# Kernel optimization log

Hardware: AMD Instinct MI355X
Metric: run time of the kernel (lower is better)

## Reference

```python
import jax, jax.numpy as jnp
import numpy as np


def group_norm(x, g, b, groups, eps=1e-5):
    # x: (B, C, H, W), PyTorch GroupNorm semantics
    B, C, H, W = x.shape
    xr = x.reshape(B, groups, -1)
    m = xr.mean(-1, keepdims=True)
    v = xr.var(-1, keepdims=True)
    xn = ((xr - m) * jax.lax.rsqrt(v + eps)).reshape(B, C, H, W)
    return xn * g[:, None, None] + b[:, None, None]


def mamba(xs, in_w, conv_w, conv_b, xproj_w, dt_w, dt_b, A_log, D, out_w):
    # Standard Mamba block: in_proj -> causal depthwise conv -> SiLU ->
    # x_proj -> softplus(dt_proj) -> selective scan -> gate -> out_proj.
    Bsz, L, d = xs.shape
    di = in_w.shape[0] // 2
    r = dt_w.shape[1]
    n = A_log.shape[1]
    K = conv_w.shape[1]
    xz = xs @ in_w.T                           # (B, L, 2*di)
    xpart, z = xz[..., :di], xz[..., di:]
    xp = jnp.pad(xpart, ((0, 0), (K - 1, 0), (0, 0)))  # causal pad
    xc = conv_b + sum(xp[:, k:k + L, :] * conv_w[:, k] for k in range(K))
    xc = jax.nn.silu(xc)
    proj = xc @ xproj_w.T                      # (B, L, r + 2n)
    dt = proj[..., :r]
    Bm = proj[..., r:r + n]
    Cm = proj[..., r + n:]
    delta = jax.nn.softplus(dt @ dt_w.T + dt_b)   # (B, L, di)
    A = -jnp.exp(A_log)                            # (di, n)
    dA = jnp.exp(jnp.einsum('bld,dn->bldn', delta, A))
    dBu = jnp.einsum('bld,bln,bld->bldn', delta, Bm, xc)

    def step(h, inp):
        dA_t, dBu_t, C_t = inp
        h = dA_t * h + dBu_t                  # (B, di, n)
        return h, jnp.einsum('bdn,bn->bd', h, C_t)

    h0 = jnp.zeros((Bsz, di, n), xs.dtype)
    _, ys = jax.lax.scan(step, h0, (jnp.moveaxis(dA, 1, 0), jnp.moveaxis(dBu, 1, 0), jnp.moveaxis(Cm, 1, 0)))
    y = jnp.moveaxis(ys, 0, 1) + D * xc
    y = y * jax.nn.silu(z)
    return y @ out_w.T


def setup_inputs() -> dict:
    def nrm(i, shape, s=0.05):
        return jax.random.normal(jax.random.fold_in(jax.random.key(0), i), shape, dtype=jnp.float32) * s

    f32 = jnp.float32
    C = 128
    di, r, n = 256, 8, 16          # spa mamba: d_model=128, expand=2
    di2, r2 = 64, 2                # spe mamba: d_model=32
    A1 = jnp.log(jnp.broadcast_to(jnp.arange(1, n + 1, dtype=f32), (di, n)))
    A2 = jnp.log(jnp.broadcast_to(jnp.arange(1, n + 1, dtype=f32), (di2, n)))
    return {
        'x': nrm(0, (2, C, 64, 64), 1.0),
        'pe_w': nrm(1, (C, C)), 'pe_b': jnp.zeros((C,), f32),
        'pe_gn_g': jnp.ones((C,), f32), 'pe_gn_b': jnp.zeros((C,), f32),
        'spa_in_w': nrm(2, (2 * di, C)),
        'spa_conv_w': nrm(3, (di, 4)), 'spa_conv_b': jnp.zeros((di,), f32),
        'spa_xproj_w': nrm(4, (r + 2 * n, di)),
        'spa_dt_w': nrm(5, (di, r)), 'spa_dt_b': jnp.full((di,), -2.0, f32),
        'spa_Alog': A1, 'spa_D': jnp.ones((di,), f32),
        'spa_out_w': nrm(6, (C, di)),
        'spa_gn_g': jnp.ones((C,), f32), 'spa_gn_b': jnp.zeros((C,), f32),
        'spe_in_w': nrm(7, (2 * di2, 32)),
        'spe_conv_w': nrm(8, (di2, 4)), 'spe_conv_b': jnp.zeros((di2,), f32),
        'spe_xproj_w': nrm(9, (r2 + 2 * n, di2)),
        'spe_dt_w': nrm(10, (di2, r2)), 'spe_dt_b': jnp.full((di2,), -2.0, f32),
        'spe_Alog': A2, 'spe_D': jnp.ones((di2,), f32),
        'spe_out_w': nrm(11, (32, di2)),
        'spe_gn_g': jnp.ones((C,), f32), 'spe_gn_b': jnp.zeros((C,), f32),
        'fuse_w': jnp.full((2,), 0.5, f32),
        'cls_w': nrm(12, (10, C)), 'cls_b': jnp.zeros((10,), f32),
        'ref_dw_w': nrm(13, (C, 1, 3, 3)),
        'ref_gn_g': jnp.ones((C,), f32), 'ref_gn_b': jnp.zeros((C,), f32),
        'ref_pw_w': nrm(14, (1, C)), 'ref_pw_b': jnp.zeros((1,), f32),
        'alpha': jnp.asarray(1e-4, f32),
    }


def reference(x, pe_w, pe_b, pe_gn_g, pe_gn_b, spa_in_w, spa_conv_w, spa_conv_b, spa_xproj_w, spa_dt_w, spa_dt_b, spa_Alog, spa_D, spa_out_w, spa_gn_g, spa_gn_b, spe_in_w, spe_conv_w, spe_conv_b, spe_xproj_w, spe_dt_w, spe_dt_b, spe_Alog, spe_D, spe_out_w, spe_gn_g, spe_gn_b, fuse_w, cls_w, cls_b, ref_dw_w, ref_gn_g, ref_gn_b, ref_pw_w, ref_pw_b, alpha):
    B, _, H, W = x.shape
    # patch embedding: 1x1 conv + GroupNorm + SiLU
    h1 = jnp.einsum('bchw,oc->bohw', x, pe_w) + pe_b[:, None, None]
    h1 = jax.nn.silu(group_norm(h1, pe_gn_g, pe_gn_b, 4))
    # SpaMamba: scan over flattened spatial tokens (B, H*W, C)
    seq = h1.transpose(0, 2, 3, 1).reshape(B, H * W, -1)
    y = mamba(seq, spa_in_w, spa_conv_w, spa_conv_b, spa_xproj_w, spa_dt_w, spa_dt_b, spa_Alog, spa_D, spa_out_w)
    y = y.reshape(B, H, W, -1).transpose(0, 3, 1, 2)
    spa = jax.nn.silu(group_norm(y, spa_gn_g, spa_gn_b, 4)) + h1
    # SpeMamba: token_num=4, group_channel_num=32, channel_num=128 (no pad)
    seq2 = h1.transpose(0, 2, 3, 1).reshape(B * H * W, 4, 32)
    y2 = mamba(seq2, spe_in_w, spe_conv_w, spe_conv_b, spe_xproj_w, spe_dt_w, spe_dt_b, spe_Alog, spe_D, spe_out_w)
    y2 = y2.reshape(B, H, W, -1).transpose(0, 3, 1, 2)
    spe = h1 + jax.nn.silu(group_norm(y2, spe_gn_g, spe_gn_b, 4))
    # attention-weighted fusion + residual (BothMamba, use_att=True)
    wts = jax.nn.softmax(fuse_w)
    feat = spa * wts[0] + spe * wts[1] + h1
    # classifier head (1x1 conv)
    logits = jnp.einsum('bchw,oc->bohw', feat, cls_w) + cls_b[:, None, None]
    # BoundaryAwareLogitRefiner
    edge = jax.lax.conv_general_dilated(feat, ref_dw_w, (1, 1), ((1, 1), (1, 1)), feature_group_count=feat.shape[1], dimension_numbers=('NCHW', 'OIHW', 'NCHW'))
    edge = jax.nn.silu(group_norm(edge, ref_gn_g, ref_gn_b, 4))
    edge = jax.nn.sigmoid(jnp.einsum('bchw,oc->bohw', edge, ref_pw_w) + ref_pw_b[:, None, None])
    local = jax.lax.reduce_window(logits, 0.0, jax.lax.add, (1, 1, 3, 3), (1, 1, 1, 1), ((0, 0), (0, 0), (1, 1), (1, 1))) / 9.0  # count_include_pad=True
    return logits + alpha * (1.0 - edge) * (local - logits)
```

## Files before the change

### kernel.cpp

```cpp
#include <hip/hip_runtime.h>
#include <math.h>

#define DEV __device__ __forceinline__

DEV float sigm(float x){ return 1.f/(1.f+__expf(-x)); }
DEV float siluf(float x){ return x * sigm(x); }
DEV float softplusf(float x){ return x > 20.f ? x : log1pf(__expf(x)); }

static constexpr float NG = 131072.0f;

static constexpr size_t WS_H1    = 0;
static constexpr size_t WS_H1PRE = 1048576;
static constexpr size_t WS_XC    = 2097152;
static constexpr size_t WS_ZSIL  = 4194304;
static constexpr size_t WS_XZ    = 6291456;
static constexpr size_t WS_DELTA = 6291456;
static constexpr size_t WS_BM    = 8388608;
static constexpr size_t WS_CM    = 8519680;
static constexpr size_t WS_LOG   = 8650752;
static constexpr size_t WS_Y     = 10485760;
static constexpr size_t WS_P     = 12582912;
static constexpr size_t WS_Q     = 13107200;
static constexpr size_t WS_HS    = 13631488;
static constexpr size_t WS_Y2    = 14155776;
static constexpr size_t WS_FEAT  = 15204352;
static constexpr size_t WS_STATS = 16252928;
static constexpr size_t WS_PEWT  = 16253056;
static constexpr size_t WS_INWT  = WS_PEWT  + 16384;
static constexpr size_t WS_OUTWT = WS_INWT  + 65536;
static constexpr size_t WS_XPWT  = WS_OUTWT + 32768;

__global__ void __launch_bounds__(256)
k_red(const float* __restrict__ part, float* __restrict__ outS, int half){
  __shared__ float red[4];
  int b = blockIdx.x >> 3, j = blockIdx.x & 7;
  float s = 0.f;
  for (int i = b*half + threadIdx.x; i < (b+1)*half; i += 256)
    s += part[(size_t)i*8 + j];
  s += __shfl_xor(s,1); s += __shfl_xor(s,2); s += __shfl_xor(s,4);
  s += __shfl_xor(s,8); s += __shfl_xor(s,16); s += __shfl_xor(s,32);
  if ((threadIdx.x & 63) == 0) red[threadIdx.x>>6] = s;
  __syncthreads();
  if (threadIdx.x == 0) outS[b*8+j] = red[0]+red[1]+red[2]+red[3];
}

__global__ void __launch_bounds__(256)
k_transpose(const float* __restrict__ pe_w, const float* __restrict__ in_w,
            const float* __restrict__ out_w, const float* __restrict__ xp_w,
            float* __restrict__ peT, float* __restrict__ inT,
            float* __restrict__ outT, float* __restrict__ xpT){
  int i0 = blockIdx.x*256 + threadIdx.x;
  int nt = gridDim.x*256;
  for (int k = i0; k < 128*128; k += nt){ int r = k >> 7, c = k & 127; peT[c*128 + r] = pe_w[k]; }
  for (int k = i0; k < 512*128; k += nt){ int r = k >> 7, c = k & 127; inT[c*512 + r] = in_w[k]; }
  for (int k = i0; k < 128*256; k += nt){ int r = k >> 8, c = k & 255; outT[c*128 + r] = out_w[k]; }
  for (int k = i0; k < 40*256;  k += nt){ int r = k >> 8, c = k & 255; xpT[c*40 + r] = xp_w[k]; }
}

__global__ void __launch_bounds__(256)
k_pe(const float* __restrict__ x, const float* __restrict__ peT,
     const float* __restrict__ pe_b, float* __restrict__ h1pre,
     float* __restrict__ part){
  __shared__ float As[16][36];
  __shared__ float Bs[16][64];
  __shared__ float red1[2][4], red2[2][4];
  int tid = threadIdx.x;
  int bx = blockIdx.x, by = blockIdx.y;
  int m0 = bx*32, n0 = by*64;
  int b = m0 >> 12, pl0 = m0 & 4095;
  int tx = tid & 15, ty = tid >> 4;
  float acc[2][4];
  #pragma unroll
  for (int i = 0; i < 2; i++)
    #pragma unroll
    for (int j = 0; j < 4; j++) acc[i][j] = 0.f;
  for (int k0 = 0; k0 < 128; k0 += 16){
    if (tid < 128){
      int k = tid >> 3, mm = (tid & 7)*4;
      float4 a = *(const float4*)(x + ((size_t)b*128 + k0+k)*4096 + pl0 + mm);
      *(float4*)&As[k][mm] = a;
    }
    {
      int k = tid >> 4, n = (tid & 15)*4;
      *(float4*)&Bs[k][n] = *(const float4*)(peT + (size_t)(k0+k)*128 + n0+n);
    }
    __syncthreads();
    #pragma unroll
    for (int k = 0; k < 16; k++){
      float2 av = *(const float2*)&As[k][ty*2];
      float4 bv = *(const float4*)&Bs[k][tx*4];
      acc[0][0] += av.x*bv.x; acc[0][1] += av.x*bv.y; acc[0][2] += av.x*bv.z; acc[0][3] += av.x*bv.w;
      acc[1][0] += av.y*bv.x; acc[1][1] += av.y*bv.y; acc[1][2] += av.y*bv.z; acc[1][3] += av.y*bv.w;
    }
    __syncthreads();
  }
  float4 bias = *(const float4*)(pe_b + n0 + tx*4);
  float s1 = 0.f, s2 = 0.f;
  #pragma unroll
  for (int i = 0; i < 2; i++){
    float4 st;
    st.x = acc[i][0]+bias.x; st.y = acc[i][1]+bias.y;
    st.z = acc[i][2]+bias.z; st.w = acc[i][3]+bias.w;
    s1 += st.x+st.y+st.z+st.w;
    s2 += st.x*st.x + st.y*st.y + st.z*st.z + st.w*st.w;
    *(float4*)(h1pre + (size_t)(m0 + ty*2 + i)*128 + n0 + tx*4) = st;
  }
  s1 += __shfl_xor(s1,1);  s2 += __shfl_xor(s2,1);
  s1 += __shfl_xor(s1,2);  s2 += __shfl_xor(s2,2);
  s1 += __shfl_xor(s1,4);  s2 += __shfl_xor(s2,4);
  s1 += __shfl_xor(s1,16); s2 += __shfl_xor(s2,16);
  s1 += __shfl_xor(s1,32); s2 += __shfl_xor(s2,32);
  int lane = tid & 63, w = tid >> 6;
  if ((lane & 55) == 0){
    int gl = (lane >> 3) & 1;
    red1[gl][w] = s1; red2[gl][w] = s2;
  }
  __syncthreads();
  if (tid < 8){
    int gg = tid >> 1, which = tid & 1;
    int gl = gg - by*2;
    float v = 0.f;
    if (gl == 0 || gl == 1){
      v = which ? (red2[gl][0]+red2[gl][1]+red2[gl][2]+red2[gl][3])
                : (red1[gl][0]+red1[gl][1]+red1[gl][2]+red1[gl][3]);
    }
    int pblk = b*256 + (bx & 127) + by*128;
    part[(size_t)pblk*8 + tid] = v;
  }
}

__global__ void __launch_bounds__(256)
k_gnsilu(const float* __restrict__ pre, const float* __restrict__ stats,
         const float* __restrict__ gw, const float* __restrict__ gb,
         float* __restrict__ outb){
  int idx = blockIdx.x*256 + threadIdx.x;
  int c = idx & 127; int pix = idx >> 7; int b = pix >> 12; int g = c >> 5;
  float s1 = stats[(b*4+g)*2], s2 = stats[(b*4+g)*2+1];
  float m = s1 * (1.f/NG);
  float v = s2 * (1.f/NG) - m*m;
  float xn = (pre[idx] - m) * rsqrtf(v + 1e-5f);
  float val = xn * gw[c] + gb[c];
  outb[idx] = siluf(val);
}

__global__ void __launch_bounds__(256)
k_xz(const float* __restrict__ h1, const float* __restrict__ inT,
     float* __restrict__ xz){
  __shared__ float As[16][68];
  __shared__ float Bs[16][64];
  int tid = threadIdx.x;
  int m0 = blockIdx.x*64, n0 = blockIdx.y*64;
  int tx = tid & 15, ty = tid >> 4;
  float acc[4][4];
  #pragma unroll
  for (int i = 0; i < 4; i++)
    #pragma unroll
    for (int j = 0; j < 4; j++) acc[i][j] = 0.f;
  for (int k0 = 0; k0 < 128; k0 += 16){
    {
      int m = tid >> 2, kk = (tid & 3)*4;
      float4 a = *(const float4*)(h1 + (size_t)(m0+m)*128 + k0+kk);
      As[kk+0][m] = a.x; As[kk+1][m] = a.y; As[kk+2][m] = a.z; As[kk+3][m] = a.w;
    }
    {
      int k = tid >> 4, n = (tid & 15)*4;
      *(float4*)&Bs[k][n] = *(const float4*)(inT + (size_t)(k0+k)*512 + n0+n);
    }
    __syncthreads();
    #pragma unroll
    for (int k = 0; k < 16; k++){
      float4 av = *(const float4*)&As[k][ty*4];
      float4 bv = *(const float4*)&Bs[k][tx*4];
      acc[0][0] += av.x*bv.x; acc[0][1] += av.x*bv.y; acc[0][2] += av.x*bv.z; acc[0][3] += av.x*bv.w;
      acc[1][0] += av.y*bv.x; acc[1][1] += av.y*bv.y; acc[1][2] += av.y*bv.z; acc[1][3] += av.y*bv.w;
      acc[2][0] += av.z*bv.x; acc[2][1] += av.z*bv.y; acc[2][2] += av.z*bv.z; acc[2][3] += av.z*bv.w;
      acc[3][0] += av.w*bv.x; acc[3][1] += av.w*bv.y; acc[3][2] += av.w*bv.z; acc[3][3] += av.w*bv.w;
    }
    __syncthreads();
  }
  #pragma unroll
  for (int i = 0; i < 4; i++){
    float4 st; st.x = acc[i][0]; st.y = acc[i][1]; st.z = acc[i][2]; st.w = acc[i][3];
    *(float4*)(xz + (size_t)(m0 + ty*4 + i)*512 + n0 + tx*4) = st;
  }
}

__global__ void __launch_bounds__(256)
k_conv(const float* __restrict__ xz, const float* __restrict__ cw,
       const float* __restrict__ cb, float* __restrict__ xc,
       float* __restrict__ zsil){
  int idx = blockIdx.x*256 + threadIdx.x;
  int d = idx & 255;
  int l = (idx >> 8) & 4095;
  int b = idx >> 20;
  float v = cb[d];
  #pragma unroll
  for (int k = 0; k < 4; k++){
    int ls = l - 3 + k;
    if (ls >= 0) v += xz[(size_t)(b*4096 + ls)*512 + d] * cw[d*4 + k];
  }
  xc[idx] = siluf(v);
  float z = xz[(size_t)(b*4096 + l)*512 + 256 + d];
  zsil[idx] = siluf(z);
}

__global__ void __launch_bounds__(256)
k_proj(const float* __restrict__ xc, const float* __restrict__ xpT,
       const float* __restrict__ dtw, const float* __restrict__ dtb,
       float* __restrict__ delta, float* __restrict__ Bm, float* __restrict__ Cm){
  __shared__ float xt[32][260];
  __shared__ float pr[32][40];
  int tid = threadIdx.x;
  int m0 = blockIdx.x * 32;
  for (int i = tid; i < 32*256; i += 256){
    int t = i >> 8, d = i & 255;
    xt[t][d] = xc[(size_t)(m0+t)*256 + d];
  }
  __syncthreads();
  {
    int t = tid >> 3, j0 = tid & 7;
    float a0=0.f,a1=0.f,a2=0.f,a3=0.f,a4=0.f;
    for (int d = 0; d < 256; d++){
      float xv = xt[t][d];
      const float* wp = &xpT[d*40 + j0];
      a0 += xv*wp[0]; a1 += xv*wp[8]; a2 += xv*wp[16]; a3 += xv*wp[24]; a4 += xv*wp[32];
    }
    pr[t][j0] = a0; pr[t][j0+8] = a1; pr[t][j0+16] = a2; pr[t][j0+24] = a3; pr[t][j0+32] = a4;
  }
  __syncthreads();
  {
    int d = tid;
    float w[8];
    #pragma unroll
    for (int r = 0; r < 8; r++) w[r] = dtw[d*8+r];
    float bd = dtb[d];
    for (int t = 0; t < 32; t++){
      float val = bd;
      #pragma unroll
      for (int r = 0; r < 8; r++) val += pr[t][r]*w[r];
      delta[(size_t)(m0+t)*256 + d] = softplusf(val);
    }
  }
  for (int i = tid; i < 512; i += 256){
    int t = i >> 4, n = i & 15;
    Bm[(size_t)(m0+t)*16 + n] = pr[t][8+n];
    Cm[(size_t)(m0+t)*16 + n] = pr[t][24+n];
  }
}

__global__ void __launch_bounds__(256)
k_scan1(const float* __restrict__ delta, const float* __restrict__ xc,
        const float* __restrict__ Bm, const float* __restrict__ Alog,
        float* __restrict__ P, float* __restrict__ Q){
  __shared__ float sd[64][16], sx[64][16], sb[64][16];
  int blk = blockIdx.x;
  int b = blk >> 10;
  int chunk = (blk >> 4) & 63;
  int dblk = blk & 15;
  int tid = threadIdx.x;
  size_t rowbase = (size_t)(b*4096 + chunk*64);
  for (int i = tid; i < 64*16; i += 256){
    int ii = i >> 4, dd = i & 15;
    sd[ii][dd] = delta[(rowbase + ii)*256 + dblk*16 + dd];
    sx[ii][dd] = xc  [(rowbase + ii)*256 + dblk*16 + dd];
    sb[ii][dd] = Bm  [(rowbase + ii)*16 + dd];
  }
  int dl = tid >> 4, n = tid & 15;
  int d = dblk*16 + dl;
  float An = -__expf(Alog[d*16 + n]);
  __syncthreads();
  float Pv = 1.f, Qv = 0.f;
  for (int i = 0; i < 64; i++){
    float dv = sd[i][dl];
    float a = __expf(dv * An);
    Qv = a*Qv + dv * sb[i][n] * sx[i][dl];
    Pv *= a;
  }
  size_t o = (size_t)(b*64+chunk)*4096 + dblk*256 + tid;
  P[o] = Pv; Q[o] = Qv;
}

__global__ void __launch_bounds__(256)
k_scan2(const float* __restrict__ P, const float* __restrict__ Q,
        float* __restrict__ hs){
  int gid = blockIdx.x*256 + threadIdx.x;
  int b = gid >> 12, dn = gid & 4095;
  float h = 0.f;
  for (int ch = 0; ch < 64; ch++){
    size_t idx = (size_t)(b*64 + ch)*4096 + dn;
    hs[idx] = h;
    h = P[idx]*h + Q[idx];
  }
}

__global__ void __launch_bounds__(256)
k_scan3(const float* __restrict__ delta, const float* __restrict__ xc,
        const float* __restrict__ Bm, const float* __restrict__ Cm,
        const float* __restrict__ zsil, const float* __restrict__ Alog,
        const float* __restrict__ Dv, const float* __restrict__ hs,
        float* __restrict__ y){
  __shared__ float sd[64][16], sx[64][16], sb[64][16], sc[64][16], sz[64][16], yt[64][16];
  int blk = blockIdx.x;
  int b = blk >> 10;
  int chunk = (blk >> 4) & 63;
  int dblk = blk & 15;
  int tid = threadIdx.x;
  size_t rowbase = (size_t)(b*4096 + chunk*64);
  for (int i = tid; i < 64*16; i += 256){
    int ii = i >> 4, dd = i & 15;
    sd[ii][dd] = delta[(rowbase + ii)*256 + dblk*16 + dd];
    sx[ii][dd] = xc  [(rowbase + ii)*256 + dblk*16 + dd];
    sz[ii][dd] = zsil[(rowbase + ii)*256 + dblk*16 + dd];
    sb[ii][dd] = Bm  [(rowbase + ii)*16 + dd];
    sc[ii][dd] = Cm  [(rowbase + ii)*16 + dd];
  }
  int dl = tid >> 4, n = tid & 15;
  int d = dblk*16 + dl;
  float An = -__expf(Alog[d*16 + n]);
  float h = hs[(size_t)(b*64+chunk)*4096 + dblk*256 + tid];
  float Dd = Dv[d];
  __syncthreads();
  for (int i = 0; i < 64; i++){
    float dv = sd[i][dl], xv = sx[i][dl];
    float a = __expf(dv * An);
    h = a*h + dv * sb[i][n] * xv;
    float ctr = h * sc[i][n];
    ctr += __shfl_xor(ctr, 1);
    ctr += __shfl_xor(ctr, 2);
    ctr += __shfl_xor(ctr, 4);
    ctr += __shfl_xor(ctr, 8);
    if (n == 0) yt[i][dl] = (ctr + Dd*xv) * sz[i][dl];
  }
  __syncthreads();
  for (int i = tid; i < 1024; i += 256){
    int ii = i >> 4, dd = i & 15;
    y[(rowbase + ii)*256 + dblk*16 + dd] = yt[ii][dd];
  }
}

__global__ void __launch_bounds__(256)
k_outproj(const float* __restrict__ y, const float* __restrict__ outT,
          float* __restrict__ yproj, float* __restrict__ part){
  __shared__ float As[16][36];
  __shared__ float Bs[16][64];
  __shared__ float red1[2][4], red2[2][4];
  int tid = threadIdx.x;
  int bx = blockIdx.x, by = blockIdx.y;
  int m0 = bx*32, n0 = by*64;
  int b = m0 >> 12;
  int tx = tid & 15, ty = tid >> 4;
  float acc[2][4];
  #pragma unroll
  for (int i = 0; i < 2; i++)
    #pragma unroll
    for (int j = 0; j < 4; j++) acc[i][j] = 0.f;
  for (int k0 = 0; k0 < 256; k0 += 16){
    if (tid < 128){
      int m = tid >> 2, kk = (tid & 3)*4;
      float4 a = *(const float4*)(y + (size_t)(m0+m)*256 + k0+kk);
      As[kk+0][m] = a.x; As[kk+1][m] = a.y; As[kk+2][m] = a.z; As[kk+3][m] = a.w;
    }
    {
      int k = tid >> 4, n = (tid & 15)*4;
      *(float4*)&Bs[k][n] = *(const float4*)(outT + (size_t)(k0+k)*128 + n0+n);
    }
    __syncthreads();
    #pragma unroll
    for (int k = 0; k < 16; k++){
      float2 av = *(const float2*)&As[k][ty*2];
      float4 bv = *(const float4*)&Bs[k][tx*4];
      acc[0][0] += av.x*bv.x; acc[0][1] += av.x*bv.y; acc[0][2] += av.x*bv.z; acc[0][3] += av.x*bv.w;
      acc[1][0] += av.y*bv.x; acc[1][1] += av.y*bv.y; acc[1][2] += av.y*bv.z; acc[1][3] += av.y*bv.w;
    }
    __syncthreads();
  }
  float s1 = 0.f, s2 = 0.f;
  #pragma unroll
  for (int i = 0; i < 2; i++){
    float4 st; st.x = acc[i][0]; st.y = acc[i][1]; st.z = acc[i][2]; st.w = acc[i][3];
    s1 += st.x+st.y+st.z+st.w;
    s2 += st.x*st.x + st.y*st.y + st.z*st.z + st.w*st.w;
    *(float4*)(yproj + (size_t)(m0 + ty*2 + i)*128 + n0 + tx*4) = st;
  }
  s1 += __shfl_xor(s1,1);  s2 += __shfl_xor(s2,1);
  s1 += __shfl_xor(s1,2);  s2 += __shfl_xor(s2,2);
  s1 += __shfl_xor(s1,4);  s2 += __shfl_xor(s2,4);
  s1 += __shfl_xor(s1,16); s2 += __shfl_xor(s2,16);
  s1 += __shfl_xor(s1,32); s2 += __shfl_xor(s2,32);
  int lane = tid & 63, w = tid >> 6;
  if ((lane & 55) == 0){
    int gl = (lane >> 3) & 1;
    red1[gl][w] = s1; red2[gl][w] = s2;
  }
  __syncthreads();
  if (tid < 8){
    int gg = tid >> 1, which = tid & 1;
    int gl = gg - by*2;
    float v = 0.f;
    if (gl == 0 || gl == 1){
      v = which ? (red2[gl][0]+red2[gl][1]+red2[gl][2]+red2[gl][3])
                : (red1[gl][0]+red1[gl][1]+red1[gl][2]+red1[gl][3]);
    }
    int pblk = b*256 + (bx & 127) + by*128;
    part[(size_t)pblk*8 + tid] = v;
  }
}

__global__ void __launch_bounds__(256)
k_spe_a(const float* __restrict__ h1, const float* __restrict__ in_w,
        const float* __restrict__ conv_w, const float* __restrict__ conv_b,
        float* __restrict__ xc2, float* __restrict__ xc2T,
        float* __restrict__ zsil2){
  __shared__ float s_in[4][128];
  int tid = threadIdx.x;
  int w = tid >> 6, lane = tid & 63;
  float wx[32], wz[32];
  {
    const float4* rx = (const float4*)(in_w + (size_t)lane*32);
    const float4* rz = (const float4*)(in_w + (size_t)(64+lane)*32);
    #pragma unroll
    for (int k = 0; k < 8; k++){
      float4 a = rx[k]; wx[k*4]=a.x; wx[k*4+1]=a.y; wx[k*4+2]=a.z; wx[k*4+3]=a.w;
      float4 b = rz[k]; wz[k*4]=b.x; wz[k*4+1]=b.y; wz[k*4+2]=b.z; wz[k*4+3]=b.w;
    }
  }
  float4 cwv = ((const float4*)conv_w)[lane];
  float cbv = conv_b[lane];
  for (int i = 0; i < 4; i++){
    int pix = blockIdx.x*16 + w*4 + i;
    float2 hv = ((const float2*)(h1 + (size_t)pix*128))[lane];
    s_in[w][2*lane] = hv.x; s_in[w][2*lane+1] = hv.y;
    float xpr[4], zs[4];
    #pragma unroll
    for (int l = 0; l < 4; l++){
      const float4* sv = (const float4*)&s_in[w][l*32];
      float ax = 0.f, az = 0.f;
      #pragma unroll
      for (int c4 = 0; c4 < 8; c4++){
        float4 v = sv[c4];
        ax += v.x*wx[c4*4] + v.y*wx[c4*4+1] + v.z*wx[c4*4+2] + v.w*wx[c4*4+3];
        az += v.x*wz[c4*4] + v.y*wz[c4*4+1] + v.z*wz[c4*4+2] + v.w*wz[c4*4+3];
      }
      xpr[l] = ax; zs[l] = siluf(az);
    }
    #pragma unroll
    for (int l = 0; l < 4; l++){
      float v = cbv;
      if (l >= 3) v += xpr[l-3]*cwv.x;
      if (l >= 2) v += xpr[l-2]*cwv.y;
      if (l >= 1) v += xpr[l-1]*cwv.z;
      v += xpr[l]*cwv.w;
      float sx = siluf(v);
      int tok = pix*4 + l;
      xc2 [(size_t)tok*64 + lane] = sx;
      xc2T[(size_t)lane*32768 + tok] = sx;
      zsil2[(size_t)tok*64 + lane] = zs[l];
    }
  }
}

__global__ void __launch_bounds__(256)
k_spe_b(const float* __restrict__ xc2T, const float* __restrict__ xpw,
        float* __restrict__ proj){
  int tok = blockIdx.x*256 + threadIdx.x;
  float xcv[64];
  #pragma unroll 64
  for (int dd = 0; dd < 64; dd++) xcv[dd] = xc2T[(size_t)dd*32768 + tok];
  float* pr = proj + (size_t)tok*36;
  #pragma unroll 2
  for (int j = 0; j < 34; j++){
    const float4* wr = (const float4*)(xpw + j*64);
    float a = 0.f;
    #pragma unroll
    for (int k = 0; k < 16; k++){
      float4 wv = wr[k];
      a += xcv[k*4]*wv.x + xcv[k*4+1]*wv.y + xcv[k*4+2]*wv.z + xcv[k*4+3]*wv.w;
    }
    pr[j] = a;
  }
}

__global__ void __launch_bounds__(256)
k_spe_c(const float* __restrict__ xc2, const float* __restrict__ zsil2,
        const float* __restrict__ proj, const float* __restrict__ dt_w,
        const float* __restrict__ dt_b, const float* __restrict__ Alog,
        const float* __restrict__ Dvec, float* __restrict__ yg){
  int tid = threadIdx.x;
  int w = tid >> 6, lane = tid & 63;
  float2 dtwv = ((const float2*)dt_w)[lane];
  float dbv = dt_b[lane], Dd = Dvec[lane];
  float An[16];
  {
    const float4* ar = (const float4*)(Alog + (size_t)lane*16);
    #pragma unroll
    for (int k = 0; k < 4; k++){
      float4 a = ar[k];
      An[k*4]   = -__expf(a.x); An[k*4+1] = -__expf(a.y);
      An[k*4+2] = -__expf(a.z); An[k*4+3] = -__expf(a.w);
    }
  }
  for (int i = 0; i < 4; i++){
    int pix = blockIdx.x*16 + w*4 + i;
    float h[16];
    #pragma unroll
    for (int n = 0; n < 16; n++) h[n] = 0.f;
    #pragma unroll
    for (int l = 0; l < 4; l++){
      int tok = pix*4 + l;
      float pj[36];
      {
        const float4* pr = (const float4*)(proj + (size_t)tok*36);
        #pragma unroll
        for (int k = 0; k < 9; k++){
          float4 v = pr[k];
          pj[k*4]=v.x; pj[k*4+1]=v.y; pj[k*4+2]=v.z; pj[k*4+3]=v.w;
        }
      }
      float xv = xc2[(size_t)tok*64 + lane];
      float zv = zsil2[(size_t)tok*64 + lane];
      float dt = softplusf(dbv + pj[0]*dtwv.x + pj[1]*dtwv.y);
      float ys = 0.f;
      #pragma unroll
      for (int n = 0; n < 16; n++){
        float a = __expf(dt * An[n]);
        h[n] = a*h[n] + dt * pj[2+n] * xv;
        ys += h[n] * pj[18+n];
      }
      yg[(size_t)tok*64 + lane] = (ys + Dd*xv) * zv;
    }
  }
}

__global__ void __launch_bounds__(256)
k_spe_d(const float* __restrict__ yg, const float* __restrict__ out_w,
        float* __restrict__ y2, float* __restrict__ part){
  __shared__ float ldsWT[64*32];
  __shared__ float bst[8];
  int tid = threadIdx.x;
  for (int i = tid; i < 2048; i += 256){
    int c2 = i >> 6, dd = i & 63;
    ldsWT[dd*32 + c2] = out_w[i];
  }
  if (tid < 8) bst[tid] = 0.f;
  __syncthreads();
  int w = tid >> 6, lane = tid & 63;
  int c2 = lane & 31, slot = lane >> 5;
  int tokbase = blockIdx.x*64 + w*16 + slot;
  float acc[8];
  #pragma unroll
  for (int i = 0; i < 8; i++) acc[i] = 0.f;
  for (int dd4 = 0; dd4 < 16; dd4++){
    float w0 = ldsWT[(dd4*4+0)*32 + c2];
    float w1 = ldsWT[(dd4*4+1)*32 + c2];
    float w2 = ldsWT[(dd4*4+2)*32 + c2];
    float w3 = ldsWT[(dd4*4+3)*32 + c2];
    #pragma unroll
    for (int i = 0; i < 8; i++){
      int tok = tokbase + 2*i;
      float4 yv = ((const float4*)(yg + (size_t)tok*64))[dd4];
      acc[i] += yv.x*w0 + yv.y*w1 + yv.z*w2 + yv.w*w3;
    }
  }
  #pragma unroll
  for (int i = 0; i < 8; i++){
    int tok = tokbase + 2*i;
    int pix = tok >> 2, l = tok & 3;
    y2[(size_t)pix*128 + l*32 + c2] = acc[i];
    float s1 = acc[i], s2 = acc[i]*acc[i];
    s1 += __shfl_xor(s1,1);  s2 += __shfl_xor(s2,1);
    s1 += __shfl_xor(s1,2);  s2 += __shfl_xor(s2,2);
    s1 += __shfl_xor(s1,4);  s2 += __shfl_xor(s2,4);
    s1 += __shfl_xor(s1,8);  s2 += __shfl_xor(s2,8);
    s1 += __shfl_xor(s1,16); s2 += __shfl_xor(s2,16);
    if (c2 == 0){
      atomicAdd(&bst[l*2+0], s1);
      atomicAdd(&bst[l*2+1], s2);
    }
  }
  __syncthreads();
  if (tid < 8) part[(size_t)blockIdx.x*8 + tid] = bst[tid];
}

__global__ void __launch_bounds__(256)
k_fuse(const float* __restrict__ h1, const float* __restrict__ yproj,
       const float* __restrict__ y2, const float* __restrict__ stats,
       const float* __restrict__ spa_g, const float* __restrict__ spa_b,
       const float* __restrict__ spe_g, const float* __restrict__ spe_b,
       const float* __restrict__ fuse_w, const float* __restrict__ cls_w,
       const float* __restrict__ cls_b, float* __restrict__ feat,
       float* __restrict__ logits){
  __shared__ float ft[2][128];
  int tid = threadIdx.x;
  int pixl = tid >> 7, c = tid & 127;
  int pix = blockIdx.x*2 + pixl;
  int b = pix >> 12, g = c >> 5;
  float m1 = stats[16 + (b*4+g)*2]   * (1.f/NG);
  float v1 = stats[16 + (b*4+g)*2+1] * (1.f/NG) - m1*m1;
  float m2 = stats[32 + (b*4+g)*2]   * (1.f/NG);
  float v2 = stats[32 + (b*4+g)*2+1] * (1.f/NG) - m2*m2;
  float h = h1[(size_t)pix*128 + c];
  float sa = siluf((yproj[(size_t)pix*128+c] - m1)*rsqrtf(v1+1e-5f)*spa_g[c] + spa_b[c]) + h;
  float sp = h + siluf((y2[(size_t)pix*128+c] - m2)*rsqrtf(v2+1e-5f)*spe_g[c] + spe_b[c]);
  float e0 = __expf(fuse_w[0]), e1 = __expf(fuse_w[1]);
  float w0 = e0/(e0+e1), w1 = e1/(e0+e1);
  float f = sa*w0 + sp*w1 + h;
  feat[(size_t)pix*128+c] = f;
  ft[pixl][c] = f;
  __syncthreads();
  if (tid < 20){
    int pl = (tid >= 10) ? 1 : 0;
    int o = tid - pl*10;
    float acc = cls_b[o];
    for (int cc = 0; cc < 128; cc++) acc += ft[pl][cc]*cls_w[o*128+cc];
    logits[(size_t)(blockIdx.x*2 + pl)*16 + o] = acc;
  }
}

__global__ void __launch_bounds__(256)
k_dw(const float* __restrict__ feat, const float* __restrict__ dww,
     float* __restrict__ epre, float* __restrict__ part){
  __shared__ float red1[4][64], red2[4][64];
  int tid = threadIdx.x;
  int pixl = tid >> 7, c = tid & 127;
  int pix = blockIdx.x*2 + pixl;
  int b = pix >> 12, p = pix & 4095, yy = p >> 6, xx = p & 63;
  float acc = 0.f;
  for (int dy = -1; dy <= 1; dy++){
    int ny = yy + dy; if (ny < 0 || ny > 63) continue;
    for (int dx = -1; dx <= 1; dx++){
      int nx = xx + dx; if (nx < 0 || nx > 63) continue;
      acc += feat[(size_t)((b<<12)|(ny<<6)|nx)*128 + c] * dww[c*9 + (dy+1)*3 + (dx+1)];
    }
  }
  epre[(size_t)pix*128 + c] = acc;
  int g = c >> 5;
  int idx = (c & 31) | (pixl << 5);
  red1[g][idx] = acc; red2[g][idx] = acc*acc;
  __syncthreads();
  int rg = tid >> 6, ridx = tid & 63;
  for (int s = 32; s >= 1; s >>= 1){
    if (ridx < s){ red1[rg][ridx] += red1[rg][ridx+s]; red2[rg][ridx] += red2[rg][ridx+s]; }
    __syncthreads();
  }
  if (ridx == 0){
    part[(size_t)blockIdx.x*8 + rg*2+0] = red1[rg][0];
    part[(size_t)blockIdx.x*8 + rg*2+1] = red2[rg][0];
  }
}

__global__ void __launch_bounds__(256)
k_final(const float* __restrict__ epre, const float* __restrict__ logits,
        const float* __restrict__ stats, const float* __restrict__ rg_g,
        const float* __restrict__ rg_b, const float* __restrict__ pw_w,
        const float* __restrict__ pw_b, const float* __restrict__ alpha,
        float* __restrict__ outp){
  __shared__ float part[4];
  __shared__ float edge_s[2];
  int tid = threadIdx.x;
  int pixl = tid >> 7, c = tid & 127;
  int pix = blockIdx.x*2 + pixl;
  int b = pix >> 12, p = pix & 4095, yy = p >> 6, xx = p & 63;
  int g = c >> 5;
  float m = stats[48 + (b*4+g)*2]   * (1.f/NG);
  float v = stats[48 + (b*4+g)*2+1] * (1.f/NG) - m*m;
  float e = epre[(size_t)pix*128+c];
  float en = siluf((e-m)*rsqrtf(v+1e-5f)*rg_g[c] + rg_b[c]);
  float pv = en * pw_w[c];
  pv += __shfl_xor(pv,1);  pv += __shfl_xor(pv,2);  pv += __shfl_xor(pv,4);
  pv += __shfl_xor(pv,8);  pv += __shfl_xor(pv,16); pv += __shfl_xor(pv,32);
  if ((tid & 63) == 0) part[tid>>6] = pv;
  __syncthreads();
  if (tid < 2) edge_s[tid] = sigm(part[tid*2] + part[tid*2+1] + pw_b[0]);
  __syncthreads();
  if (c < 10){
    float ed = edge_s[pixl];
    int o = c;
    float lg = logits[(size_t)pix*16 + o];
    float loc = 0.f;
    for (int dy = -1; dy <= 1; dy++){
      int ny = yy+dy; if (ny < 0 || ny > 63) continue;
      for (int dx = -1; dx <= 1; dx++){
        int nx = xx+dx; if (nx < 0 || nx > 63) continue;
        loc += logits[(size_t)((b<<12)|(ny<<6)|nx)*16 + o];
      }
    }
    loc *= (1.f/9.f);
    outp[(size_t)((b*10+o)<<12) + p] = lg + alpha[0]*(1.f-ed)*(loc - lg);
  }
}

extern "C" void kernel_launch(void* const* d_in, const int* in_sizes, int n_in,
                              void* d_out, int out_size, void* d_ws, size_t ws_size,
                              hipStream_t stream){
  const float* x          = (const float*)d_in[0];
  const float* pe_w       = (const float*)d_in[1];
  const float* pe_b       = (const float*)d_in[2];
  const float* pe_gn_g    = (const float*)d_in[3];
  const float* pe_gn_b    = (const float*)d_in[4];
  const float* spa_in_w   = (const float*)d_in[5];
  const float* spa_conv_w = (const float*)d_in[6];
  const float* spa_conv_b = (const float*)d_in[7];
  const float* spa_xproj_w= (const float*)d_in[8];
  const float* spa_dt_w   = (const float*)d_in[9];
  const float* spa_dt_b   = (const float*)d_in[10];
  const float* spa_Alog   = (const float*)d_in[11];
  const float* spa_D      = (const float*)d_in[12];
  const float* spa_out_w  = (const float*)d_in[13];
  const float* spa_gn_g   = (const float*)d_in[14];
  const float* spa_gn_b   = (const float*)d_in[15];
  const float* spe_in_w   = (const float*)d_in[16];
  const float* spe_conv_w = (const float*)d_in[17];
  const float* spe_conv_b = (const float*)d_in[18];
  const float* spe_xproj_w= (const float*)d_in[19];
  const float* spe_dt_w   = (const float*)d_in[20];
  const float* spe_dt_b   = (const float*)d_in[21];
  const float* spe_Alog   = (const float*)d_in[22];
  const float* spe_D      = (const float*)d_in[23];
  const float* spe_out_w  = (const float*)d_in[24];
  const float* spe_gn_g   = (const float*)d_in[25];
  const float* spe_gn_b   = (const float*)d_in[26];
  const float* fuse_w     = (const float*)d_in[27];
  const float* cls_w      = (const float*)d_in[28];
  const float* cls_b      = (const float*)d_in[29];
  const float* ref_dw_w   = (const float*)d_in[30];
  const float* ref_gn_g   = (const float*)d_in[31];
  const float* ref_gn_b   = (const float*)d_in[32];
  const float* ref_pw_w   = (const float*)d_in[33];
  const float* ref_pw_b   = (const float*)d_in[34];
  const float* alpha      = (const float*)d_in[35];
  float* ws  = (float*)d_ws;
  float* out = (float*)d_out;

  float* partPE  = ws + WS_Y;
  float* partSPA = ws + WS_HS;
  float* partSPE = ws + WS_Q;
  float* partDW  = ws + WS_P;
  float* xc2   = ws + WS_XC;
  float* xc2T  = ws + WS_ZSIL;
  float* zsil2 = ws + WS_DELTA;
  float* proj  = ws + WS_BM;
  float* yg    = ws + WS_Y;

  k_transpose<<<64,256,0,stream>>>(pe_w, spa_in_w, spa_out_w, spa_xproj_w,
      ws+WS_PEWT, ws+WS_INWT, ws+WS_OUTWT, ws+WS_XPWT);
  k_pe<<<dim3(256,2),256,0,stream>>>(x, ws+WS_PEWT, pe_b, ws+WS_H1PRE, partPE);
  k_red<<<16,256,0,stream>>>(partPE, ws+WS_STATS+0, 256);
  k_gnsilu<<<4096,256,0,stream>>>(ws+WS_H1PRE, ws+WS_STATS, pe_gn_g, pe_gn_b, ws+WS_H1);
  k_xz<<<dim3(128,8),256,0,stream>>>(ws+WS_H1, ws+WS_INWT, ws+WS_XZ);
  k_conv<<<8192,256,0,stream>>>(ws+WS_XZ, spa_conv_w, spa_conv_b, ws+WS_XC, ws+WS_ZSIL);
  k_proj<<<256,256,0,stream>>>(ws+WS_XC, ws+WS_XPWT, spa_dt_w, spa_dt_b,
      ws+WS_DELTA, ws+WS_BM, ws+WS_CM);
  k_scan1<<<2048,256,0,stream>>>(ws+WS_DELTA, ws+WS_XC, ws+WS_BM, spa_Alog, ws+WS_P, ws+WS_Q);
  k_scan2<<<32,256,0,stream>>>(ws+WS_P, ws+WS_Q, ws+WS_HS);
  k_scan3<<<2048,256,0,stream>>>(ws+WS_DELTA, ws+WS_XC, ws+WS_BM, ws+WS_CM,
      ws+WS_ZSIL, spa_Alog, spa_D, ws+WS_HS, ws+WS_Y);
  k_outproj<<<dim3(256,2),256,0,stream>>>(ws+WS_Y, ws+WS_OUTWT, ws+WS_H1PRE, partSPA);
  k_red<<<16,256,0,stream>>>(partSPA, ws+WS_STATS+16, 256);
  k_spe_a<<<512,256,0,stream>>>(ws+WS_H1, spe_in_w, spe_conv_w, spe_conv_b,
      xc2, xc2T, zsil2);
  k_spe_b<<<128,256,0,stream>>>(xc2T, spe_xproj_w, proj);
  k_spe_c<<<512,256,0,stream>>>(xc2, zsil2, proj, spe_dt_w, spe_dt_b,
      spe_Alog, spe_D, yg);
  k_spe_d<<<512,256,0,stream>>>(yg, spe_out_w, ws+WS_Y2, partSPE);
  k_red<<<16,256,0,stream>>>(partSPE, ws+WS_STATS+32, 256);
  k_fuse<<<4096,256,0,stream>>>(ws+WS_H1, ws+WS_H1PRE, ws+WS_Y2, ws+WS_STATS,
      spa_gn_g, spa_gn_b, spe_gn_g, spe_gn_b, fuse_w, cls_w, cls_b,
      ws+WS_FEAT, ws+WS_LOG);
  k_dw<<<4096,256,0,stream>>>(ws+WS_FEAT, ref_dw_w, ws+WS_Y, partDW);
  k_red<<<16,256,0,stream>>>(partDW, ws+WS_STATS+48, 2048);
  k_final<<<4096,256,0,stream>>>(ws+WS_Y, ws+WS_LOG, ws+WS_STATS,
      ref_gn_g, ref_gn_b, ref_pw_w, ref_pw_b, alpha, out);
  (void)in_sizes; (void)n_in; (void)out_size; (void)ws_size;
}
```

Baseline: 407.9 us.

## Fuse GroupNorm into in_proj, move z-SiLU to GEMM, restructure selective scan

The GroupNorm+SiLU kernel is folded into the in_proj GEMM's A-tile load, and SiLU(z) is computed in the GEMM epilogue instead of in the conv kernel. The chunked scan is reorganised so each thread owns one channel with all 16 states in registers. This drops the shared-memory staging and shuffle reductions, and the chunk-prefix pass becomes a parallel wavefront shuffle scan. Scan kernels now launch only 128 blocks, which lowers occupancy and parallelism. Normalisation is also recomputed redundantly across the 8 N-tiles.

```diff
diff --git a/kernel.cpp b/kernel.cpp
--- a/kernel.cpp
+++ b/kernel.cpp
@@ -130,22 +130,10 @@
 }
 
 __global__ void __launch_bounds__(256)
-k_gnsilu(const float* __restrict__ pre, const float* __restrict__ stats,
-         const float* __restrict__ gw, const float* __restrict__ gb,
-         float* __restrict__ outb){
-  int idx = blockIdx.x*256 + threadIdx.x;
-  int c = idx & 127; int pix = idx >> 7; int b = pix >> 12; int g = c >> 5;
-  float s1 = stats[(b*4+g)*2], s2 = stats[(b*4+g)*2+1];
-  float m = s1 * (1.f/NG);
-  float v = s2 * (1.f/NG) - m*m;
-  float xn = (pre[idx] - m) * rsqrtf(v + 1e-5f);
-  float val = xn * gw[c] + gb[c];
-  outb[idx] = siluf(val);
-}
-
-__global__ void __launch_bounds__(256)
-k_xz(const float* __restrict__ h1, const float* __restrict__ inT,
-     float* __restrict__ xz){
+k_xz(const float* __restrict__ h1pre, const float* __restrict__ inT,
+     const float* __restrict__ stats, const float* __restrict__ gng,
+     const float* __restrict__ gnb, float* __restrict__ h1,
+     float* __restrict__ xz, float* __restrict__ zsil){
   __shared__ float As[16][68];
   __shared__ float Bs[16][64];
   int tid = threadIdx.x;
@@ -159,8 +147,21 @@
   for (int k0 = 0; k0 < 128; k0 += 16){
     {
       int m = tid >> 2, kk = (tid & 3)*4;
-      float4 a = *(const float4*)(h1 + (size_t)(m0+m)*128 + k0+kk);
-      As[kk+0][m] = a.x; As[kk+1][m] = a.y; As[kk+2][m] = a.z; As[kk+3][m] = a.w;
+      int pixm = m0 + m, c0 = k0 + kk;
+      int bb = pixm >> 12, g = c0 >> 5;
+      float4 a = *(const float4*)(h1pre + (size_t)pixm*128 + c0);
+      float mu = stats[(bb*4+g)*2] * (1.f/NG);
+      float var = stats[(bb*4+g)*2+1] * (1.f/NG) - mu*mu;
+      float rs = rsqrtf(var + 1e-5f);
+      float4 gg = *(const float4*)(gng + c0);
+      float4 gb = *(const float4*)(gnb + c0);
+      float4 v;
+      v.x = siluf((a.x-mu)*rs*gg.x + gb.x);
+      v.y = siluf((a.y-mu)*rs*gg.y + gb.y);
+      v.z = siluf((a.z-mu)*rs*gg.z + gb.z);
+      v.w = siluf((a.w-mu)*rs*gg.w + gb.w);
+      As[kk+0][m] = v.x; As[kk+1][m] = v.y; As[kk+2][m] = v.z; As[kk+3][m] = v.w;
+      if (blockIdx.y == 0) *(float4*)(h1 + (size_t)pixm*128 + c0) = v;
     }
     {
       int k = tid >> 4, n = (tid & 15)*4;
@@ -178,17 +179,26 @@
     }
     __syncthreads();
   }
-  #pragma unroll
-  for (int i = 0; i < 4; i++){
-    float4 st; st.x = acc[i][0]; st.y = acc[i][1]; st.z = acc[i][2]; st.w = acc[i][3];
-    *(float4*)(xz + (size_t)(m0 + ty*4 + i)*512 + n0 + tx*4) = st;
+  if (n0 < 256){
+    #pragma unroll
+    for (int i = 0; i < 4; i++){
+      float4 st; st.x = acc[i][0]; st.y = acc[i][1]; st.z = acc[i][2]; st.w = acc[i][3];
+      *(float4*)(xz + (size_t)(m0 + ty*4 + i)*512 + n0 + tx*4) = st;
+    }
+  } else {
+    #pragma unroll
+    for (int i = 0; i < 4; i++){
+      float4 st;
+      st.x = siluf(acc[i][0]); st.y = siluf(acc[i][1]);
+      st.z = siluf(acc[i][2]); st.w = siluf(acc[i][3]);
+      *(float4*)(zsil + (size_t)(m0 + ty*4 + i)*256 + (n0-256) + tx*4) = st;
+    }
   }
 }
 
 __global__ void __launch_bounds__(256)
 k_conv(const float* __restrict__ xz, const float* __restrict__ cw,
-       const float* __restrict__ cb, float* __restrict__ xc,
-       float* __restrict__ zsil){
+       const float* __restrict__ cb, float* __restrict__ xc){
   int idx = blockIdx.x*256 + threadIdx.x;
   int d = idx & 255;
   int l = (idx >> 8) & 4095;
@@ -200,8 +210,6 @@
     if (ls >= 0) v += xz[(size_t)(b*4096 + ls)*512 + d] * cw[d*4 + k];
   }
   xc[idx] = siluf(v);
-  float z = xz[(size_t)(b*4096 + l)*512 + 256 + d];
-  zsil[idx] = siluf(z);
 }
 
 __global__ void __launch_bounds__(256)
@@ -218,14 +226,20 @@
   }
   __syncthreads();
   {
-    int t = tid >> 3, j0 = tid & 7;
-    float a0=0.f,a1=0.f,a2=0.f,a3=0.f,a4=0.f;
+    int t = tid >> 3, q = tid & 7;
+    bool extra = (q < 2);
+    float4 a0 = {0.f,0.f,0.f,0.f}, a1 = {0.f,0.f,0.f,0.f};
     for (int d = 0; d < 256; d++){
       float xv = xt[t][d];
-      const float* wp = &xpT[d*40 + j0];
-      a0 += xv*wp[0]; a1 += xv*wp[8]; a2 += xv*wp[16]; a3 += xv*wp[24]; a4 += xv*wp[32];
-    }
-    pr[t][j0] = a0; pr[t][j0+8] = a1; pr[t][j0+16] = a2; pr[t][j0+24] = a3; pr[t][j0+32] = a4;
+      float4 w0 = *(const float4*)(xpT + (size_t)d*40 + q*4);
+      a0.x += xv*w0.x; a0.y += xv*w0.y; a0.z += xv*w0.z; a0.w += xv*w0.w;
+      if (extra){
+        float4 w1 = *(const float4*)(xpT + (size_t)d*40 + 32 + q*4);
+        a1.x += xv*w1.x; a1.y += xv*w1.y; a1.z += xv*w1.z; a1.w += xv*w1.w;
+      }
+    }
+    *(float4*)&pr[t][q*4] = a0;
+    if (extra) *(float4*)&pr[t][32+q*4] = a1;
   }
   __syncthreads();
   {
@@ -252,45 +266,67 @@
 k_scan1(const float* __restrict__ delta, const float* __restrict__ xc,
         const float* __restrict__ Bm, const float* __restrict__ Alog,
         float* __restrict__ P, float* __restrict__ Q){
-  __shared__ float sd[64][16], sx[64][16], sb[64][16];
   int blk = blockIdx.x;
-  int b = blk >> 10;
-  int chunk = (blk >> 4) & 63;
-  int dblk = blk & 15;
-  int tid = threadIdx.x;
-  size_t rowbase = (size_t)(b*4096 + chunk*64);
-  for (int i = tid; i < 64*16; i += 256){
-    int ii = i >> 4, dd = i & 15;
-    sd[ii][dd] = delta[(rowbase + ii)*256 + dblk*16 + dd];
-    sx[ii][dd] = xc  [(rowbase + ii)*256 + dblk*16 + dd];
-    sb[ii][dd] = Bm  [(rowbase + ii)*16 + dd];
-  }
-  int dl = tid >> 4, n = tid & 15;
-  int d = dblk*16 + dl;
-  float An = -__expf(Alog[d*16 + n]);
-  __syncthreads();
-  float Pv = 1.f, Qv = 0.f;
-  for (int i = 0; i < 64; i++){
-    float dv = sd[i][dl];
-    float a = __expf(dv * An);
-    Qv = a*Qv + dv * sb[i][n] * sx[i][dl];
-    Pv *= a;
-  }
-  size_t o = (size_t)(b*64+chunk)*4096 + dblk*256 + tid;
-  P[o] = Pv; Q[o] = Qv;
+  int b = blk >> 6, chunk = blk & 63;
+  int d = threadIdx.x;
+  float An[16];
+  {
+    const float4* ar = (const float4*)(Alog + (size_t)d*16);
+    #pragma unroll
+    for (int k = 0; k < 4; k++){
+      float4 a = ar[k];
+      An[k*4]   = -__expf(a.x); An[k*4+1] = -__expf(a.y);
+      An[k*4+2] = -__expf(a.z); An[k*4+3] = -__expf(a.w);
+    }
+  }
+  float Pv[16], Qv[16];
+  #pragma unroll
+  for (int n = 0; n < 16; n++){ Pv[n] = 1.f; Qv[n] = 0.f; }
+  size_t row0 = (size_t)(b*4096 + chunk*64);
+  for (int l = 0; l < 64; l++){
+    size_t r = row0 + l;
+    float dv = delta[r*256 + d];
+    float xv = xc[r*256 + d];
+    const float4* bmr = (const float4*)(Bm + r*16);
+    float4 b0 = bmr[0], b1 = bmr[1], b2 = bmr[2], b3 = bmr[3];
+    float bm[16] = {b0.x,b0.y,b0.z,b0.w, b1.x,b1.y,b1.z,b1.w,
+                    b2.x,b2.y,b2.z,b2.w, b3.x,b3.y,b3.z,b3.w};
+    float dBx = dv * xv;
+    #pragma unroll
+    for (int n = 0; n < 16; n++){
+      float a = __expf(dv * An[n]);
+      Qv[n] = a*Qv[n] + bm[n]*dBx;
+      Pv[n] *= a;
+    }
+  }
+  float* Pp = P + (size_t)blk*4096 + d*16;
+  float* Qp = Q + (size_t)blk*4096 + d*16;
+  #pragma unroll
+  for (int k = 0; k < 4; k++){
+    float4 pv; pv.x = Pv[k*4]; pv.y = Pv[k*4+1]; pv.z = Pv[k*4+2]; pv.w = Pv[k*4+3];
+    float4 qv; qv.x = Qv[k*4]; qv.y = Qv[k*4+1]; qv.z = Qv[k*4+2]; qv.w = Qv[k*4+3];
+    *(float4*)(Pp + k*4) = pv;
+    *(float4*)(Qp + k*4) = qv;
+  }
 }
 
 __global__ void __launch_bounds__(256)
 k_scan2(const float* __restrict__ P, const float* __restrict__ Q,
         float* __restrict__ hs){
-  int gid = blockIdx.x*256 + threadIdx.x;
-  int b = gid >> 12, dn = gid & 4095;
-  float h = 0.f;
-  for (int ch = 0; ch < 64; ch++){
-    size_t idx = (size_t)(b*64 + ch)*4096 + dn;
-    hs[idx] = h;
-    h = P[idx]*h + Q[idx];
-  }
+  int chain = blockIdx.x*4 + (threadIdx.x >> 6);
+  int lane = threadIdx.x & 63;
+  int b = chain >> 12, dn = chain & 4095;
+  size_t idx = (size_t)(b*64 + lane)*4096 + dn;
+  float p = P[idx], q = Q[idx];
+  #pragma unroll
+  for (int off = 1; off < 64; off <<= 1){
+    float pp = __shfl_up(p, off);
+    float qp = __shfl_up(q, off);
+    if (lane >= off){ q = p*qp + q; p = p*pp; }
+  }
+  float hprev = __shfl_up(q, 1);
+  if (lane == 0) hprev = 0.f;
+  hs[idx] = hprev;
 }
 
 __global__ void __launch_bounds__(256)
@@ -299,42 +335,52 @@
         const float* __restrict__ zsil, const float* __restrict__ Alog,
         const float* __restrict__ Dv, const float* __restrict__ hs,
         float* __restrict__ y){
-  __shared__ float sd[64][16], sx[64][16], sb[64][16], sc[64][16], sz[64][16], yt[64][16];
   int blk = blockIdx.x;
-  int b = blk >> 10;
-  int chunk = (blk >> 4) & 63;
-  int dblk = blk & 15;
-  int tid = threadIdx.x;
-  size_t rowbase = (size_t)(b*4096 + chunk*64);
-  for (int i = tid; i < 64*16; i += 256){
-    int ii = i >> 4, dd = i & 15;
-    sd[ii][dd] = delta[(rowbase + ii)*256 + dblk*16 + dd];
-    sx[ii][dd] = xc  [(rowbase + ii)*256 + dblk*16 + dd];
-    sz[ii][dd] = zsil[(rowbase + ii)*256 + dblk*16 + dd];
-    sb[ii][dd] = Bm  [(rowbase + ii)*16 + dd];
-    sc[ii][dd] = Cm  [(rowbase + ii)*16 + dd];
-  }
-  int dl = tid >> 4, n = tid & 15;
-  int d = dblk*16 + dl;
-  float An = -__expf(Alog[d*16 + n]);
-  float h = hs[(size_t)(b*64+chunk)*4096 + dblk*256 + tid];
+  int b = blk >> 6, chunk = blk & 63;
+  int d = threadIdx.x;
+  float An[16];
+  {
+    const float4* ar = (const float4*)(Alog + (size_t)d*16);
+    #pragma unroll
+    for (int k = 0; k < 4; k++){
+      float4 a = ar[k];
+      An[k*4]   = -__expf(a.x); An[k*4+1] = -__expf(a.y);
+      An[k*4+2] = -__expf(a.z); An[k*4+3] = -__expf(a.w);
+    }
+  }
+  float h[16];
+  {
+    const float4* hr = (const float4*)(hs + (size_t)blk*4096 + d*16);
+    #pragma unroll
+    for (int k = 0; k < 4; k++){
+      float4 v = hr[k];
+      h[k*4] = v.x; h[k*4+1] = v.y; h[k*4+2] = v.z; h[k*4+3] = v.w;
+    }
+  }
   float Dd = Dv[d];
-  __syncthreads();
-  for (int i = 0; i < 64; i++){
-    float dv = sd[i][dl], xv = sx[i][dl];
-    float a = __expf(dv * An);
-    h = a*h + dv * sb[i][n] * xv;
-    float ctr = h * sc[i][n];
-    ctr += __shfl_xor(ctr, 1);
-    ctr += __shfl_xor(ctr, 2);
-    ctr += __shfl_xor(ctr, 4);
-    ctr += __shfl_xor(ctr, 8);
-    if (n == 0) yt[i][dl] = (ctr + Dd*xv) * sz[i][dl];
-  }
-  __syncthreads();
-  for (int i = tid; i < 1024; i += 256){
-    int ii = i >> 4, dd = i & 15;
-    y[(rowbase + ii)*256 + dblk*16 + dd] = yt[ii][dd];
+  size_t row0 = (size_t)(b*4096 + chunk*64);
+  for (int l = 0; l < 64; l++){
+    size_t r = row0 + l;
+    float dv = delta[r*256 + d];
+    float xv = xc[r*256 + d];
+    float zv = zsil[r*256 + d];
+    const float4* bmr = (const float4*)(Bm + r*16);
+    float4 b0 = bmr[0], b1 = bmr[1], b2 = bmr[2], b3 = bmr[3];
+    float bm[16] = {b0.x,b0.y,b0.z,b0.w, b1.x,b1.y,b1.z,b1.w,
+                    b2.x,b2.y,b2.z,b2.w, b3.x,b3.y,b3.z,b3.w};
+    const float4* cmr = (const float4*)(Cm + r*16);
+    float4 c0 = cmr[0], c1 = cmr[1], c2 = cmr[2], c3 = cmr[3];
+    float cm[16] = {c0.x,c0.y,c0.z,c0.w, c1.x,c1.y,c1.z,c1.w,
+                    c2.x,c2.y,c2.z,c2.w, c3.x,c3.y,c3.z,c3.w};
+    float dBx = dv * xv;
+    float ys = 0.f;
+    #pragma unroll
+    for (int n = 0; n < 16; n++){
+      float a = __expf(dv * An[n]);
+      h[n] = a*h[n] + bm[n]*dBx;
+      ys += h[n]*cm[n];
+    }
+    y[r*256 + d] = (ys + Dd*xv) * zv;
   }
 }
 
@@ -745,14 +791,15 @@
       ws+WS_PEWT, ws+WS_INWT, ws+WS_OUTWT, ws+WS_XPWT);
   k_pe<<<dim3(256,2),256,0,stream>>>(x, ws+WS_PEWT, pe_b, ws+WS_H1PRE, partPE);
   k_red<<<16,256,0,stream>>>(partPE, ws+WS_STATS+0, 256);
-  k_gnsilu<<<4096,256,0,stream>>>(ws+WS_H1PRE, ws+WS_STATS, pe_gn_g, pe_gn_b, ws+WS_H1);
-  k_xz<<<dim3(128,8),256,0,stream>>>(ws+WS_H1, ws+WS_INWT, ws+WS_XZ);
-  k_conv<<<8192,256,0,stream>>>(ws+WS_XZ, spa_conv_w, spa_conv_b, ws+WS_XC, ws+WS_ZSIL);
+  k_xz<<<dim3(128,8),256,0,stream>>>(ws+WS_H1PRE, ws+WS_INWT, ws+WS_STATS,
+      pe_gn_g, pe_gn_b, ws+WS_H1, ws+WS_XZ, ws+WS_ZSIL);
+  k_conv<<<8192,256,0,stream>>>(ws+WS_XZ, spa_conv_w, spa_conv_b, ws+WS_XC);
   k_proj<<<256,256,0,stream>>>(ws+WS_XC, ws+WS_XPWT, spa_dt_w, spa_dt_b,
       ws+WS_DELTA, ws+WS_BM, ws+WS_CM);
-  k_scan1<<<2048,256,0,stream>>>(ws+WS_DELTA, ws+WS_XC, ws+WS_BM, spa_Alog, ws+WS_P, ws+WS_Q);
-  k_scan2<<<32,256,0,stream>>>(ws+WS_P, ws+WS_Q, ws+WS_HS);
-  k_scan3<<<2048,256,0,stream>>>(ws+WS_DELTA, ws+WS_XC, ws+WS_BM, ws+WS_CM,
+  k_scan1<<<128,256,0,stream>>>(ws+WS_DELTA, ws+WS_XC, ws+WS_BM, spa_Alog,
+      ws+WS_P, ws+WS_Q);
+  k_scan2<<<2048,256,0,stream>>>(ws+WS_P, ws+WS_Q, ws+WS_HS);
+  k_scan3<<<128,256,0,stream>>>(ws+WS_DELTA, ws+WS_XC, ws+WS_BM, ws+WS_CM,
       ws+WS_ZSIL, spa_Alog, spa_D, ws+WS_HS, ws+WS_Y);
   k_outproj<<<dim3(256,2),256,0,stream>>>(ws+WS_Y, ws+WS_OUTWT, ws+WS_H1PRE, partSPA);
   k_red<<<16,256,0,stream>>>(partSPA, ws+WS_STATS+16, 256);
```

New measurement: 493.0 us. 20.9% more time.
